# Kernel tuning notes

Measured on AMD Instinct MI355X. Metric: run time of the kernel, lower is better.

The kernel has to match this reference:

```python
import jax, jax.numpy as jnp
import numpy as np

N = 100000   # num_nodes
R = 200      # num_relations
DIM = 200    # hidden dim (in = out for every layer)
B = 30       # num_bases
L = 2        # num_layers
E = 800000   # num_edges


def setup_inputs() -> dict:
    key = jax.random.key(0)
    ks = jax.random.split(key, 7)
    edge_index = jax.random.randint(ks[0], (2, E), 0, N)
    edge_type = jax.random.randint(ks[1], (E,), 0, R)
    s = 1.0 / np.sqrt(DIM)
    emb = jax.random.normal(ks[2], (N, DIM), jnp.float32)
    comp = jax.random.normal(ks[3], (L, R, B), jnp.float32) * (1.0 / np.sqrt(B))
    bases = jax.random.normal(ks[4], (L, B, DIM, DIM), jnp.float32) * s
    root = jax.random.normal(ks[5], (L, DIM, DIM), jnp.float32) * s
    bias = jnp.zeros((L, DIM), jnp.float32)
    return dict(edge_index=edge_index, edge_type=edge_type, emb=emb,
                comp=comp, bases=bases, root=root, bias=bias)


def _rgcn_layer(x, src, dst, etype, comp_l, bases_l, root_l, bias_l):
    # Basis decomposition: W_r = sum_b comp[r, b] * bases[b]
    # msg_e = x[src_e] @ W_{etype_e}  computed as sum over bases (B is small & fixed)
    x_src = x[src]                      # [E, DIM] gather
    c = comp_l[etype]                   # [E, B] per-edge basis coefficients

    def body(acc, bc):
        basis_b, c_b = bc               # [DIM, DIM], [E]
        return acc + c_b[:, None] * (x_src @ basis_b), None

    acc0 = jnp.zeros((x_src.shape[0], root_l.shape[1]), x.dtype)
    msg, _ = jax.lax.scan(body, acc0, (bases_l, jnp.swapaxes(c, 0, 1)))  # [E, DIM]

    # PyG RGCNConv mean aggregation: normalize by in-degree per (dst node, relation)
    comb = dst * R + etype
    deg = jax.ops.segment_sum(jnp.ones((etype.shape[0],), x.dtype), comb,
                              num_segments=N * R)
    norm = 1.0 / jnp.maximum(deg[comb], 1.0)                             # [E]

    agg = jax.ops.segment_sum(msg * norm[:, None], dst, num_segments=N)  # [N, DIM]
    return agg + x @ root_l + bias_l


def reference(edge_index, edge_type, emb, comp, bases, root, bias):
    src, dst = edge_index[0], edge_index[1]
    x = emb
    for l in range(L):
        x = jax.nn.relu(_rgcn_layer(x, src, dst, edge_type,
                                    comp[l], bases[l], root[l], bias[l]))
        # dropout is identity in eval mode (deterministic reference)
    return x
```

## Files before the change

### kernel.cpp

```cpp
#include <hip/hip_runtime.h>
#include <hip/hip_bf16.h>
#include <stdint.h>

#define NN 100000
#define RR 200
#define DD 200
#define BB 30
#define LL 2
#define EE 800000

#define KP 224
#define NP 208
#define XP 208
#define AP 232
#define TE 128
#define MSGP 200
#define MAXTILES 6700
#define MAXNC 16
#define NPART 256
#define EPB ((EE + NPART - 1) / NPART)

using bf16x8 = __attribute__((ext_vector_type(8))) short;
using f32x4  = __attribute__((ext_vector_type(4))) float;

#define OFF_NORM   0ull
#define OFF_SORT   3200000ull
#define OFF_CNT    6400000ull
#define OFF_XB     6404096ull
#define OFF_WT     48004096ull
#define OFF_ROOTT  66640896ull
#define OFF_CTL    66734080ull
#define OFF_POS    66799616ull
#define OFF_DSTCNT 69999616ull
#define OFF_DSTST  70399616ull
#define OFF_CUR    70799632ull
#define OFF_BLKH   71199632ull
#define OFF_MSG    74476432ull

static __device__ __forceinline__ short f2bf(float v) {
    union { __hip_bfloat16 h; short s; } u;
    u.h = __float2bfloat16(v);
    return u.s;
}

__global__ void kCount(const int* __restrict__ ei, const int* __restrict__ et,
                       unsigned int* __restrict__ deg8, int* __restrict__ dstCnt, int big) {
    int e = blockIdx.x * 256 + threadIdx.x;
    if (e >= EE) return;
    int d = ei[EE + e];
    int t = et[e];
    int comb = d * RR + t;
    atomicAdd(&deg8[comb >> 2], 1u << ((comb & 3) * 8));
    if (big) atomicAdd(&dstCnt[d], 1);
}

__global__ void kScanBlk(const int* __restrict__ dstCnt, int* __restrict__ dstStart,
                         int* __restrict__ blkSum) {
    __shared__ int s[256];
    int t = threadIdx.x, i = blockIdx.x * 256 + t;
    int v = (i < NN) ? dstCnt[i] : 0;
    s[t] = v;
    __syncthreads();
    #pragma unroll
    for (int off = 1; off < 256; off <<= 1) {
        int x = (t >= off) ? s[t - off] : 0;
        __syncthreads();
        s[t] += x;
        __syncthreads();
    }
    if (i < NN) dstStart[i] = s[t] - v;
    if (t == 255) blkSum[blockIdx.x] = s[255];
}
__global__ void kScanTop(int* __restrict__ blkSum, int nblk) {
    __shared__ int s[512];
    int t = threadIdx.x;
    int v = (t < nblk) ? blkSum[t] : 0;
    s[t] = v;
    __syncthreads();
    #pragma unroll
    for (int off = 1; off < 512; off <<= 1) {
        int x = (t >= off) ? s[t - off] : 0;
        __syncthreads();
        s[t] += x;
        __syncthreads();
    }
    if (t < nblk) blkSum[t] = s[t] - v;
}
__global__ void kScanAdd(const int* __restrict__ dstCnt, int* __restrict__ dstStart,
                         const int* __restrict__ blkSum) {
    int i = blockIdx.x * 256 + threadIdx.x;
    if (i >= NN) return;
    int v = dstStart[i] + blkSum[blockIdx.x];
    dstStart[i] = v;
    if (i == NN - 1) dstStart[NN] = v + dstCnt[i];
}

__global__ void kChunk(const int* __restrict__ dstStart, int* __restrict__ bS,
                       int* __restrict__ cesS, int NC, int T) {
    int tid = threadIdx.x;
    if (tid > NC) return;
    int v;
    if (tid == NC) v = NN;
    else if (tid == 0) v = 0;
    else {
        int target = tid * T;
        int lo = 0, hi = NN;
        while (lo < hi) {
            int mid = (lo + hi) >> 1;
            if (dstStart[mid] >= target) hi = mid; else lo = mid + 1;
        }
        v = lo;
    }
    bS[tid] = v;
    cesS[tid] = dstStart[v];
}

__global__ __launch_bounds__(256) void kHist(const int* __restrict__ ei,
        const int* __restrict__ et, const int* __restrict__ bS,
        int* __restrict__ blockHist, int NC) {
    __shared__ int hist[MAXNC * RR];
    __shared__ int bsh[MAXNC + 1];
    int tid = threadIdx.x, b = blockIdx.x;
    int NB = NC * RR;
    if (tid <= NC) bsh[tid] = bS[tid];
    for (int i = tid; i < NB; i += 256) hist[i] = 0;
    __syncthreads();
    int ebeg = b * EPB, eend = min(EE, ebeg + EPB);
    for (int e = ebeg + tid; e < eend; e += 256) {
        int d = ei[EE + e];
        int t = et[e];
        int c = 0;
        for (int j = 1; j < NC; ++j) if (d >= bsh[j]) c = j;
        atomicAdd(&hist[c * RR + t], 1);
    }
    __syncthreads();
    for (int i = tid; i < NB; i += 256)
        blockHist[(size_t)b * NB + i] = hist[i];
}

__global__ __launch_bounds__(256) void kScanP(int* __restrict__ blockHist,
                                              int* __restrict__ cntB, int NB) {
    __shared__ int s[256];
    int t = threadIdx.x, k = blockIdx.x;
    int v = blockHist[(size_t)t * NB + k];
    s[t] = v;
    __syncthreads();
    #pragma unroll
    for (int off = 1; off < 256; off <<= 1) {
        int x = (t >= off) ? s[t - off] : 0;
        __syncthreads();
        s[t] += x;
        __syncthreads();
    }
    blockHist[(size_t)t * NB + k] = s[t] - v;
    if (t == 255) cntB[k] = s[255];
}

__global__ void kScanB(const int* __restrict__ cntB, int* __restrict__ relStartB,
                       int* __restrict__ cursorB, int* __restrict__ tileOffB, int nb) {
    __shared__ int c[MAXNC * RR];
    __shared__ int rs[MAXNC * RR + 1];
    __shared__ int to[MAXNC * RR + 1];
    int tid = threadIdx.x;
    for (int i = tid; i < nb; i += 256) c[i] = cntB[i];
    __syncthreads();
    if (tid == 0) {
        int s = 0, ts = 0;
        for (int i = 0; i < nb; ++i) {
            rs[i] = s; to[i] = ts;
            s += c[i];
            ts += (c[i] + TE - 1) / TE;
        }
        rs[nb] = s; to[nb] = ts;
    }
    __syncthreads();
    for (int i = tid; i <= nb; i += 256) {
        relStartB[i] = rs[i];
        tileOffB[i]  = to[i];
        if (i < nb) cursorB[i] = rs[i];
    }
}

__global__ __launch_bounds__(256) void kPart(const int* __restrict__ ei,
        const int* __restrict__ et, const unsigned int* __restrict__ deg8,
        const int* __restrict__ bS, const int* __restrict__ relStartB,
        const int* __restrict__ blockHist, const int* __restrict__ dstStart,
        int* __restrict__ cur, float* __restrict__ norm, int* __restrict__ sortedE,
        int* __restrict__ posDst, int NC) {
    __shared__ int curL[MAXNC * RR];
    __shared__ int bsh[MAXNC + 1];
    int tid = threadIdx.x, b = blockIdx.x;
    int NB = NC * RR;
    if (tid <= NC) bsh[tid] = bS[tid];
    for (int i = tid; i < NB; i += 256)
        curL[i] = relStartB[i] + blockHist[(size_t)b * NB + i];
    __syncthreads();
    int ebeg = b * EPB, eend = min(EE, ebeg + EPB);
    for (int e = ebeg + tid; e < eend; e += 256) {
        int d = ei[EE + e];
        int t = et[e];
        int comb = d * RR + t;
        unsigned int deg = (deg8[comb >> 2] >> ((comb & 3) * 8)) & 0xffu;
        norm[e] = 1.0f / (float)(deg ? deg : 1u);
        int c = 0;
        for (int j = 1; j < NC; ++j) if (d >= bsh[j]) c = j;
        int pos = atomicAdd(&curL[c * RR + t], 1);
        sortedE[pos] = e;
        posDst[e] = dstStart[d] + atomicAdd(&cur[d], 1);
    }
}

__global__ void kCountB(const int* __restrict__ ei, const int* __restrict__ et,
                        const int* __restrict__ bS, int* __restrict__ cntB, int NC) {
    __shared__ int bsh[MAXNC + 1];
    if (threadIdx.x <= NC) bsh[threadIdx.x] = bS[threadIdx.x];
    __syncthreads();
    int e = blockIdx.x * 256 + threadIdx.x;
    if (e >= EE) return;
    int d = ei[EE + e];
    int t = et[e];
    int c = 0;
    for (int j = 1; j < NC; ++j) if (d >= bsh[j]) c = j;
    atomicAdd(&cntB[c * RR + t], 1);
}

__global__ void kNormScatter(const int* __restrict__ ei, const int* __restrict__ et,
                             const unsigned int* __restrict__ deg8, const int* __restrict__ bS,
                             int* __restrict__ cursorB, const int* __restrict__ dstStart,
                             int* __restrict__ cur, float* __restrict__ norm,
                             int* __restrict__ sortedE, int* __restrict__ posDst,
                             int NC, int big) {
    __shared__ int bsh[MAXNC + 1];
    if (threadIdx.x <= NC) bsh[threadIdx.x] = bS[threadIdx.x];
    __syncthreads();
    int e = blockIdx.x * 256 + threadIdx.x;
    if (e >= EE) return;
    int d = ei[EE + e];
    int t = et[e];
    int comb = d * RR + t;
    unsigned int deg = (deg8[comb >> 2] >> ((comb & 3) * 8)) & 0xffu;
    norm[e] = 1.0f / (float)(deg ? deg : 1u);
    int c = 0;
    for (int j = 1; j < NC; ++j) if (d >= bsh[j]) c = j;
    int pos = atomicAdd(&cursorB[c * RR + t], 1);
    sortedE[pos] = e;
    if (big) posDst[e] = dstStart[d] + atomicAdd(&cur[d], 1);
}

__global__ void kConvert(const float* __restrict__ x, short* __restrict__ xb, int doRelu) {
    int idx = blockIdx.x * 256 + threadIdx.x;
    if (idx >= NN * XP) return;
    int i = idx / XP, col = idx - i * XP;
    float v = 0.0f;
    if (col < DD) {
        v = x[i * DD + col];
        if (doRelu) v = fmaxf(v, 0.0f);
    }
    xb[idx] = (col < DD) ? f2bf(v) : (short)0;
}

__global__ void kRelu(float* __restrict__ y) {
    int idx = blockIdx.x * 256 + threadIdx.x;
    if (idx < NN * DD) y[idx] = fmaxf(y[idx], 0.0f);
}

__global__ __launch_bounds__(256) void kW(const float* __restrict__ comp,
                                          const float* __restrict__ bases,
                                          short* __restrict__ Wt) {
    int kt = blockIdx.x;
    int ng = blockIdx.y;
    int tid = threadIdx.x;
    int k = kt * 32 + (tid & 31);
    int n = ng * 8 + (tid >> 5);
    bool live = (k < DD) && (n < DD);
    float vb[BB];
    #pragma unroll
    for (int b = 0; b < BB; ++b)
        vb[b] = live ? bases[((size_t)b * DD + k) * DD + n] : 0.0f;
    size_t wo = (size_t)n * KP + k;
    for (int r = 0; r < RR; ++r) {
        float a = 0.0f;
        #pragma unroll
        for (int b = 0; b < BB; ++b) a += comp[r * BB + b] * vb[b];
        Wt[(size_t)r * (NP * KP) + wo] = f2bf(a);
    }
}

__global__ void kRootT(const float* __restrict__ root, short* __restrict__ rootT) {
    int idx = blockIdx.x * 256 + threadIdx.x;
    if (idx >= NP * KP) return;
    int n = idx / KP, k = idx - n * KP;
    rootT[idx] = (n < DD && k < DD) ? f2bf(root[k * DD + n]) : (short)0;
}

template<int F0, int NF>
__device__ __forceinline__ void gemmHalf2(const short* As, const short* bCol,
                                          int arow0, int arow1, int kg,
                                          f32x4* acc0, f32x4* acc1) {
    #pragma unroll
    for (int f = 0; f < NF; ++f) {
        acc0[f] = (f32x4){0.f, 0.f, 0.f, 0.f};
        acc1[f] = (f32x4){0.f, 0.f, 0.f, 0.f};
    }
    bf16x8 bb[2][NF];
    #pragma unroll
    for (int f = 0; f < NF; ++f)
        bb[0][f] = *(const bf16x8*)(bCol + (size_t)(F0 + f) * 16 * KP);
    #pragma unroll
    for (int kc = 0; kc < 7; ++kc) {
        if (kc < 6) {
            #pragma unroll
            for (int f = 0; f < NF; ++f)
                bb[(kc + 1) & 1][f] = *(const bf16x8*)(bCol + (size_t)(F0 + f) * 16 * KP + (kc + 1) * 32);
        }
        bf16x8 a0 = *(const bf16x8*)(&As[arow0 * AP + kc * 32 + kg]);
        bf16x8 a1 = *(const bf16x8*)(&As[arow1 * AP + kc * 32 + kg]);
        #pragma unroll
        for (int f = 0; f < NF; ++f) {
            acc0[f] = __builtin_amdgcn_mfma_f32_16x16x32_bf16(a0, bb[kc & 1][f], acc0[f], 0, 0, 0);
            acc1[f] = __builtin_amdgcn_mfma_f32_16x16x32_bf16(a1, bb[kc & 1][f], acc1[f], 0, 0, 0);
        }
    }
}

__global__ __launch_bounds__(256) void kRootGemm(const short* __restrict__ xb,
        const short* __restrict__ rootT, const float* __restrict__ bias,
        float* __restrict__ y) {
    __shared__ short As[TE * AP];
    int i0 = blockIdx.x * TE;
    int tid = threadIdx.x;
    int rowL = tid >> 1, sub = tid & 1;
    int i = i0 + rowL;
    for (int c = sub; c < 29; c += 2) {
        int4 v = make_int4(0, 0, 0, 0);
        if (i < NN && c < 26) v = *(const int4*)(xb + (size_t)i * XP + c * 8);
        *(int4*)(&As[rowL * AP + c * 8]) = v;
    }
    __syncthreads();
    int lane = tid & 63, wave = tid >> 6;
    int arow0 = wave * 32 + (lane & 15);
    int arow1 = arow0 + 16;
    int kg = (lane >> 4) * 8;
    const short* bCol = rootT + (lane & 15) * KP + kg;
    int colLane = lane & 15;
    int rbase = i0 + wave * 32 + (lane >> 4) * 4;
    {
        f32x4 acc0[7], acc1[7];
        gemmHalf2<0, 7>(As, bCol, arow0, arow1, kg, acc0, acc1);
        #pragma unroll
        for (int f = 0; f < 7; ++f) {
            int col = f * 16 + colLane;
            float bv = bias[col];
            #pragma unroll
            for (int j = 0; j < 4; ++j) {
                int r0 = rbase + j, r1 = rbase + 16 + j;
                if (r0 < NN) y[(size_t)r0 * DD + col] = acc0[f][j] + bv;
                if (r1 < NN) y[(size_t)r1 * DD + col] = acc1[f][j] + bv;
            }
        }
    }
    {
        f32x4 acc0[6], acc1[6];
        gemmHalf2<7, 6>(As, bCol, arow0, arow1, kg, acc0, acc1);
        #pragma unroll
        for (int f = 0; f < 6; ++f) {
            int col = (7 + f) * 16 + colLane;
            if (col < DD) {
                float bv = bias[col];
                #pragma unroll
                for (int j = 0; j < 4; ++j) {
                    int r0 = rbase + j, r1 = rbase + 16 + j;
                    if (r0 < NN) y[(size_t)r0 * DD + col] = acc0[f][j] + bv;
                    if (r1 < NN) y[(size_t)r1 * DD + col] = acc1[f][j] + bv;
                }
            }
        }
    }
}

template<int MODE>
__global__ __launch_bounds__(256) void kMsg(const int* __restrict__ ei,
        const short* __restrict__ xb, const short* __restrict__ Wt,
        const int* __restrict__ relStartB, const int* __restrict__ tileOffB,
        const int* __restrict__ sortedE, const float* __restrict__ norm,
        const int* __restrict__ posDst, const int* __restrict__ cesS,
        float* __restrict__ y, short* __restrict__ msg, int c) {
    __shared__ short As[TE * AP];
    __shared__ int   posS[TE];
    __shared__ float normS[TE];
    int tbase = tileOffB[c * RR];
    int tend  = tileOffB[(c + 1) * RR];
    int tileIdx = tbase + blockIdx.x;
    if (tileIdx >= tend) return;
    int lo = c * RR, hi = (c + 1) * RR;
    while (hi - lo > 1) {
        int mid = (lo + hi) >> 1;
        if (tileOffB[mid] <= tileIdx) lo = mid; else hi = mid;
    }
    int bkt = lo;
    int r = bkt - c * RR;
    int eBase = relStartB[bkt] + (tileIdx - tileOffB[bkt]) * TE;
    int eEnd  = relStartB[bkt + 1];
    int tid = threadIdx.x;
    int rowL = tid >> 1, sub = tid & 1;
    int eIdx = eBase + rowL;
    bool valid = eIdx < eEnd;
    int eid = valid ? sortedE[eIdx] : 0;
    if (sub == 0) {
        normS[rowL] = valid ? norm[eid] : 0.0f;
        if (MODE == 0) posS[rowL] = valid ? (posDst[eid] - cesS[c]) : -1;
        else           posS[rowL] = valid ? ei[EE + eid] : -1;
    }
    int srcRow = valid ? ei[eid] : 0;
    for (int cc = sub; cc < 29; cc += 2) {
        int4 v = make_int4(0, 0, 0, 0);
        if (valid && cc < 26) v = *(const int4*)(xb + (size_t)srcRow * XP + cc * 8);
        *(int4*)(&As[rowL * AP + cc * 8]) = v;
    }
    __syncthreads();
    int lane = tid & 63, wave = tid >> 6;
    int arow0 = wave * 32 + (lane & 15);
    int arow1 = arow0 + 16;
    int kg = (lane >> 4) * 8;
    const short* bCol = Wt + (size_t)r * (NP * KP) + (lane & 15) * KP + kg;
    int colLane = lane & 15;
    int rL0 = wave * 32 + (lane >> 4) * 4;
    {
        f32x4 acc0[7], acc1[7];
        gemmHalf2<0, 7>(As, bCol, arow0, arow1, kg, acc0, acc1);
        #pragma unroll
        for (int j = 0; j < 4; ++j) {
            #pragma unroll
            for (int m = 0; m < 2; ++m) {
                int rl = rL0 + m * 16 + j;
                float nm = normS[rl];
                int ps = posS[rl];
                if (ps >= 0) {
                    #pragma unroll
                    for (int f = 0; f < 7; ++f) {
                        int col = f * 16 + colLane;
                        float val = (m ? acc1[f][j] : acc0[f][j]) * nm;
                        if (MODE == 0) msg[(size_t)ps * MSGP + col] = f2bf(val);
                        else           atomicAdd(&y[(size_t)ps * DD + col], val);
                    }
                }
            }
        }
    }
    {
        f32x4 acc0[6], acc1[6];
        gemmHalf2<7, 6>(As, bCol, arow0, arow1, kg, acc0, acc1);
        #pragma unroll
        for (int j = 0; j < 4; ++j) {
            #pragma unroll
            for (int m = 0; m < 2; ++m) {
                int rl = rL0 + m * 16 + j;
                float nm = normS[rl];
                int ps = posS[rl];
                if (ps >= 0) {
                    #pragma unroll
                    for (int f = 0; f < 6; ++f) {
                        int col = (7 + f) * 16 + colLane;
                        if (col < DD) {
                            float val = (m ? acc1[f][j] : acc0[f][j]) * nm;
                            if (MODE == 0) msg[(size_t)ps * MSGP + col] = f2bf(val);
                            else           atomicAdd(&y[(size_t)ps * DD + col], val);
                        }
                    }
                }
            }
        }
    }
}

__global__ __launch_bounds__(256) void kAgg(const short* __restrict__ msg,
        const int* __restrict__ dstStart, const int* __restrict__ bS,
        const int* __restrict__ cesS, float* __restrict__ y, int c) {
    int wv = threadIdx.x >> 6, lane = threadIdx.x & 63;
    int b0 = bS[c], b1 = bS[c + 1];
    int ces = cesS[c];
    int gw = blockIdx.x * 4 + wv;
    int nw = gridDim.x * 4;
    for (int d = b0 + gw; d < b1; d += nw) {
        int s = dstStart[d] - ces, e = dstStart[d + 1] - ces;
        float a0 = 0.f, a1 = 0.f, a2 = 0.f, a3 = 0.f;
        if (lane < 50) {
            for (int j = s; j < e; ++j) {
                int2 v = *(const int2*)(msg + (size_t)j * MSGP + lane * 4);
                unsigned u0 = (unsigned)v.x, u1 = (unsigned)v.y;
                a0 += __uint_as_float(u0 << 16);
                a1 += __uint_as_float(u0 & 0xffff0000u);
                a2 += __uint_as_float(u1 << 16);
                a3 += __uint_as_float(u1 & 0xffff0000u);
            }
            int colBase = lane * 4;
            float4 rv = *(const float4*)(y + (size_t)d * DD + colBase);
            float4 o;
            o.x = fmaxf(rv.x + a0, 0.f);
            o.y = fmaxf(rv.y + a1, 0.f);
            o.z = fmaxf(rv.z + a2, 0.f);
            o.w = fmaxf(rv.w + a3, 0.f);
            *(float4*)(y + (size_t)d * DD + colBase) = o;
        }
    }
}

extern "C" void kernel_launch(void* const* d_in, const int* in_sizes, int n_in,
                              void* d_out, int out_size, void* d_ws, size_t ws_size,
                              hipStream_t stream) {
    (void)in_sizes; (void)n_in; (void)out_size;
    const int*   ei    = (const int*)d_in[0];
    const int*   et    = (const int*)d_in[1];
    const float* emb   = (const float*)d_in[2];
    const float* comp  = (const float*)d_in[3];
    const float* bases = (const float*)d_in[4];
    const float* root  = (const float*)d_in[5];
    const float* bias  = (const float*)d_in[6];
    float* y = (float*)d_out;
    char* ws = (char*)d_ws;
    float* norm    = (float*)(ws + OFF_NORM);
    int*   sortedE = (int*)(ws + OFF_SORT);
    short* xb      = (short*)(ws + OFF_XB);
    short* Wt      = (short*)(ws + OFF_WT);
    short* rootT   = (short*)(ws + OFF_ROOTT);
    int*   posDst  = (int*)(ws + OFF_POS);
    int*   dstCnt  = (int*)(ws + OFF_DSTCNT);
    int*   dstStart= (int*)(ws + OFF_DSTST);
    int*   cur     = (int*)(ws + OFF_CUR);
    int*   blockHist = (int*)(ws + OFF_BLKH);
    short* msg     = (short*)(ws + OFF_MSG);
    unsigned int* deg8 = (unsigned int*)(ws + OFF_XB);

    int NC = 0;
    long long T = EE;
    for (int cc = 1; cc <= MAXNC; ++cc) {
        long long t = (EE + cc - 1) / cc;
        if ((unsigned long long)ws_size >= OFF_MSG + (unsigned long long)(t + 64) * (MSGP * 2)) {
            NC = cc; T = t; break;
        }
    }
    int big = (NC > 0) ? 1 : 0;
    if (!big) { NC = 1; T = EE; }

    int *cntB, *relStartB, *cursorB, *tileOffB, *bS, *cesS, *blkSum;
    if (big) {
        int* ctl = (int*)(ws + OFF_CTL);
        cntB = ctl; relStartB = ctl + 3328; cursorB = ctl + 6656;
        tileOffB = ctl + 9984; bS = ctl + 13312; cesS = ctl + 13360; blkSum = ctl + 13440;
    } else {
        int* ctl = (int*)(ws + OFF_CNT);
        cntB = ctl; relStartB = ctl + 256; cursorB = ctl + 512;
        tileOffB = ctl + 768; bS = ctl + 976; cesS = ctl + 992; blkSum = ctl + 1000;
    }

    const int NBLK = (NN + 255) / 256;

    hipMemsetAsync(deg8, 0, (size_t)NN * RR, stream);
    if (big) {
        hipMemsetAsync(dstCnt, 0, (size_t)NN * 4, stream);
        hipMemsetAsync(cur, 0, (size_t)NN * 4, stream);
    } else {
        hipMemsetAsync((void*)cntB, 0, 4096, stream);
    }

    kCount<<<(EE + 255) / 256, 256, 0, stream>>>(ei, et, deg8, dstCnt, big);
    if (big) {
        kScanBlk<<<NBLK, 256, 0, stream>>>(dstCnt, dstStart, blkSum);
        kScanTop<<<1, 512, 0, stream>>>(blkSum, NBLK);
        kScanAdd<<<NBLK, 256, 0, stream>>>(dstCnt, dstStart, blkSum);
        kChunk<<<1, 64, 0, stream>>>(dstStart, bS, cesS, NC, (int)T);
        kHist<<<NPART, 256, 0, stream>>>(ei, et, bS, blockHist, NC);
        kScanP<<<NC * RR, 256, 0, stream>>>(blockHist, cntB, NC * RR);
        kScanB<<<1, 256, 0, stream>>>(cntB, relStartB, cursorB, tileOffB, NC * RR);
        kPart<<<NPART, 256, 0, stream>>>(ei, et, deg8, bS, relStartB, blockHist,
                                         dstStart, cur, norm, sortedE, posDst, NC);
    } else {
        kCountB<<<(EE + 255) / 256, 256, 0, stream>>>(ei, et, bS, cntB, NC);
        kScanB<<<1, 256, 0, stream>>>(cntB, relStartB, cursorB, tileOffB, NC * RR);
        kNormScatter<<<(EE + 255) / 256, 256, 0, stream>>>(ei, et, deg8, bS, cursorB,
                                                           dstStart, cur, norm, sortedE,
                                                           posDst, NC, big);
    }
    kConvert<<<(NN * XP + 255) / 256, 256, 0, stream>>>(emb, xb, 0);

    int Gmsg = (int)((T + TE - 1) / TE) + RR + 4;
    for (int l = 0; l < LL; ++l) {
        kW<<<dim3(7, 26), 256, 0, stream>>>(comp + l * RR * BB,
                                            bases + (size_t)l * BB * DD * DD, Wt);
        kRootT<<<(NP * KP + 255) / 256, 256, 0, stream>>>(root + l * DD * DD, rootT);
        kRootGemm<<<(NN + TE - 1) / TE, 256, 0, stream>>>(xb, rootT, bias + l * DD, y);
        if (big) {
            for (int c = 0; c < NC; ++c) {
                kMsg<0><<<Gmsg, 256, 0, stream>>>(ei, xb, Wt, relStartB, tileOffB,
                                                  sortedE, norm, posDst, cesS, y, msg, c);
                kAgg<<<2048, 256, 0, stream>>>(msg, dstStart, bS, cesS, y, c);
            }
            if (l == 0)
                kConvert<<<(NN * XP + 255) / 256, 256, 0, stream>>>(y, xb, 0);
        } else {
            kMsg<1><<<MAXTILES, 256, 0, stream>>>(ei, xb, Wt, relStartB, tileOffB,
                                                  sortedE, norm, posDst, cesS, y, msg, 0);
            if (l == 0) kConvert<<<(NN * XP + 255) / 256, 256, 0, stream>>>(y, xb, 1);
            else        kRelu<<<(NN * DD + 255) / 256, 256, 0, stream>>>(y);
        }
    }
}
```

Before: 1.541 ms.

## Load message GEMM A-operand directly from global into registers with 64-edge tiles

The per-relation message kernel no longer stages gathered source rows in LDS. Each wave loads its 16 gathered rows straight into MFMA A registers, and the edge tile shrinks from 128 to 64 so padded tiles waste less work. The bf16 node-feature row pitch is padded to 224 so the full K range can be read without bounds checks, and the partition count is halved with the workspace offsets and chunk limits recomputed to match. This removes the LDS round trip and the block barrier, but each lane now does uncoalesced global gathers and the B-matrix weight loads are reused across fewer rows per block.

After: 1.616 ms. +4.8%, slower.

```diff
diff --git a/kernel.cpp b/kernel.cpp
--- a/kernel.cpp
+++ b/kernel.cpp
@@ -11,13 +11,14 @@
 
 #define KP 224
 #define NP 208
-#define XP 208
+#define XP 224
 #define AP 232
-#define TE 128
+#define TE 64
+#define RT 128
 #define MSGP 200
-#define MAXTILES 6700
-#define MAXNC 16
-#define NPART 256
+#define MAXTILES 12700
+#define MAXNC 24
+#define NPART 128
 #define EPB ((EE + NPART - 1) / NPART)
 
 using bf16x8 = __attribute__((ext_vector_type(8))) short;
@@ -27,15 +28,14 @@
 #define OFF_SORT   3200000ull
 #define OFF_CNT    6400000ull
 #define OFF_XB     6404096ull
-#define OFF_WT     48004096ull
-#define OFF_ROOTT  66640896ull
-#define OFF_CTL    66734080ull
-#define OFF_POS    66799616ull
-#define OFF_DSTCNT 69999616ull
-#define OFF_DSTST  70399616ull
-#define OFF_CUR    70799632ull
-#define OFF_BLKH   71199632ull
-#define OFF_MSG    74476432ull
+#define OFF_WT     51204096ull
+#define OFF_ROOTT  69840896ull
+#define OFF_CTL    69934080ull
+#define OFF_POS    70065152ull
+#define OFF_DSTCNT 73265152ull
+#define OFF_DSTST  73665152ull
+#define OFF_CUR    74065184ull
+#define OFF_BLKH   74465184ull
 
 static __device__ __forceinline__ short f2bf(float v) {
     union { __hip_bfloat16 h; short s; } u;
@@ -138,22 +138,22 @@
         blockHist[(size_t)b * NB + i] = hist[i];
 }
 
-__global__ __launch_bounds__(256) void kScanP(int* __restrict__ blockHist,
+__global__ __launch_bounds__(128) void kScanP(int* __restrict__ blockHist,
                                               int* __restrict__ cntB, int NB) {
-    __shared__ int s[256];
+    __shared__ int s[NPART];
     int t = threadIdx.x, k = blockIdx.x;
     int v = blockHist[(size_t)t * NB + k];
     s[t] = v;
     __syncthreads();
     #pragma unroll
-    for (int off = 1; off < 256; off <<= 1) {
+    for (int off = 1; off < NPART; off <<= 1) {
         int x = (t >= off) ? s[t - off] : 0;
         __syncthreads();
         s[t] += x;
         __syncthreads();
     }
     blockHist[(size_t)t * NB + k] = s[t] - v;
-    if (t == 255) cntB[k] = s[255];
+    if (t == NPART - 1) cntB[k] = s[NPART - 1];
 }
 
 __global__ void kScanB(const int* __restrict__ cntB, int* __restrict__ relStartB,
@@ -326,14 +326,14 @@
 __global__ __launch_bounds__(256) void kRootGemm(const short* __restrict__ xb,
         const short* __restrict__ rootT, const float* __restrict__ bias,
         float* __restrict__ y) {
-    __shared__ short As[TE * AP];
-    int i0 = blockIdx.x * TE;
+    __shared__ short As[RT * AP];
+    int i0 = blockIdx.x * RT;
     int tid = threadIdx.x;
     int rowL = tid >> 1, sub = tid & 1;
     int i = i0 + rowL;
-    for (int c = sub; c < 29; c += 2) {
+    for (int c = sub; c < 28; c += 2) {
         int4 v = make_int4(0, 0, 0, 0);
-        if (i < NN && c < 26) v = *(const int4*)(xb + (size_t)i * XP + c * 8);
+        if (i < NN) v = *(const int4*)(xb + (size_t)i * XP + c * 8);
         *(int4*)(&As[rowL * AP + c * 8]) = v;
     }
     __syncthreads();
@@ -385,9 +385,6 @@
         const int* __restrict__ sortedE, const float* __restrict__ norm,
         const int* __restrict__ posDst, const int* __restrict__ cesS,
         float* __restrict__ y, short* __restrict__ msg, int c) {
-    __shared__ short As[TE * AP];
-    __shared__ int   posS[TE];
-    __shared__ float normS[TE];
     int tbase = tileOffB[c * RR];
     int tend  = tileOffB[(c + 1) * RR];
     int tileIdx = tbase + blockIdx.x;
@@ -397,75 +394,96 @@
         int mid = (lo + hi) >> 1;
         if (tileOffB[mid] <= tileIdx) lo = mid; else hi = mid;
     }
-    int bkt = lo;
-    int r = bkt - c * RR;
-    int eBase = relStartB[bkt] + (tileIdx - tileOffB[bkt]) * TE;
-    int eEnd  = relStartB[bkt + 1];
-    int tid = threadIdx.x;
-    int rowL = tid >> 1, sub = tid & 1;
-    int eIdx = eBase + rowL;
-    bool valid = eIdx < eEnd;
-    int eid = valid ? sortedE[eIdx] : 0;
-    if (sub == 0) {
-        normS[rowL] = valid ? norm[eid] : 0.0f;
-        if (MODE == 0) posS[rowL] = valid ? (posDst[eid] - cesS[c]) : -1;
-        else           posS[rowL] = valid ? ei[EE + eid] : -1;
-    }
-    int srcRow = valid ? ei[eid] : 0;
-    for (int cc = sub; cc < 29; cc += 2) {
-        int4 v = make_int4(0, 0, 0, 0);
-        if (valid && cc < 26) v = *(const int4*)(xb + (size_t)srcRow * XP + cc * 8);
-        *(int4*)(&As[rowL * AP + cc * 8]) = v;
-    }
-    __syncthreads();
-    int lane = tid & 63, wave = tid >> 6;
-    int arow0 = wave * 32 + (lane & 15);
-    int arow1 = arow0 + 16;
+    int r = lo - c * RR;
+    int eBase = relStartB[lo] + (tileIdx - tileOffB[lo]) * TE;
+    int eEnd  = relStartB[lo + 1];
+    int tid = threadIdx.x, lane = tid & 63, wave = tid >> 6;
+    int stripe = wave * 16;
     int kg = (lane >> 4) * 8;
-    const short* bCol = Wt + (size_t)r * (NP * KP) + (lane & 15) * KP + kg;
     int colLane = lane & 15;
-    int rL0 = wave * 32 + (lane >> 4) * 4;
+    int eIdxA = eBase + stripe + colLane;
+    int eidA = sortedE[min(eIdxA, eEnd - 1)];
+    int srcA = ei[eidA];
+    const short* aRow = xb + (size_t)srcA * XP;
+    bf16x8 a[7];
+    #pragma unroll
+    for (int kc = 0; kc < 7; ++kc)
+        a[kc] = *(const bf16x8*)(aRow + kc * 32 + kg);
+    int rbase = stripe + (lane >> 4) * 4;
+    int psv[4]; float nmv[4];
+    #pragma unroll
+    for (int j = 0; j < 4; ++j) {
+        int eI = eBase + rbase + j;
+        bool v = eI < eEnd;
+        int eid = v ? sortedE[eI] : 0;
+        nmv[j] = v ? norm[eid] : 0.0f;
+        if (MODE == 0) psv[j] = v ? (posDst[eid] - cesS[c]) : -1;
+        else           psv[j] = v ? ei[EE + eid] : -1;
+    }
+    const short* bCol = Wt + (size_t)r * (NP * KP) + colLane * KP + kg;
     {
-        f32x4 acc0[7], acc1[7];
-        gemmHalf2<0, 7>(As, bCol, arow0, arow1, kg, acc0, acc1);
+        f32x4 acc[7];
+        #pragma unroll
+        for (int f = 0; f < 7; ++f) acc[f] = (f32x4){0.f, 0.f, 0.f, 0.f};
+        bf16x8 bb[2][7];
+        #pragma unroll
+        for (int f = 0; f < 7; ++f)
+            bb[0][f] = *(const bf16x8*)(bCol + (size_t)f * 16 * KP);
+        #pragma unroll
+        for (int kc = 0; kc < 7; ++kc) {
+            if (kc < 6) {
+                #pragma unroll
+                for (int f = 0; f < 7; ++f)
+                    bb[(kc + 1) & 1][f] = *(const bf16x8*)(bCol + (size_t)f * 16 * KP + (kc + 1) * 32);
+            }
+            #pragma unroll
+            for (int f = 0; f < 7; ++f)
+                acc[f] = __builtin_amdgcn_mfma_f32_16x16x32_bf16(a[kc], bb[kc & 1][f], acc[f], 0, 0, 0);
+        }
         #pragma unroll
         for (int j = 0; j < 4; ++j) {
+            int ps = psv[j]; float nm = nmv[j];
+            if (ps >= 0) {
+                #pragma unroll
+                for (int f = 0; f < 7; ++f) {
+                    int col = f * 16 + colLane;
+                    float val = acc[f][j] * nm;
+                    if (MODE == 0) msg[(size_t)ps * MSGP + col] = f2bf(val);
+                    else           atomicAdd(&y[(size_t)ps * DD + col], val);
+                }
+            }
+        }
+    }
+    {
+        f32x4 acc[6];
+        #pragma unroll
+        for (int f = 0; f < 6; ++f) acc[f] = (f32x4){0.f, 0.f, 0.f, 0.f};
+        bf16x8 bb[2][6];
+        #pragma unroll
+        for (int f = 0; f < 6; ++f)
+            bb[0][f] = *(const bf16x8*)(bCol + (size_t)(7 + f) * 16 * KP);
+        #pragma unroll
+        for (int kc = 0; kc < 7; ++kc) {
+            if (kc < 6) {
+                #pragma unroll
+                for (int f = 0; f < 6; ++f)
+                    bb[(kc + 1) & 1][f] = *(const bf16x8*)(bCol + (size_t)(7 + f) * 16 * KP + (kc + 1) * 32);
+            }
             #pragma unroll
-            for (int m = 0; m < 2; ++m) {
-                int rl = rL0 + m * 16 + j;
-                float nm = normS[rl];
-                int ps = posS[rl];
-                if (ps >= 0) {
-                    #pragma unroll
-                    for (int f = 0; f < 7; ++f) {
-                        int col = f * 16 + colLane;
-                        float val = (m ? acc1[f][j] : acc0[f][j]) * nm;
+            for (int f = 0; f < 6; ++f)
+                acc[f] = __builtin_amdgcn_mfma_f32_16x16x32_bf16(a[kc], bb[kc & 1][f], acc[f], 0, 0, 0);
+        }
+        #pragma unroll
+        for (int j = 0; j < 4; ++j) {
+            int ps = psv[j]; float nm = nmv[j];
+            if (ps >= 0) {
+                #pragma unroll
+                for (int f = 0; f < 6; ++f) {
+                    int col = (7 + f) * 16 + colLane;
+                    if (col < DD) {
+                        float val = acc[f][j] * nm;
                         if (MODE == 0) msg[(size_t)ps * MSGP + col] = f2bf(val);
                         else           atomicAdd(&y[(size_t)ps * DD + col], val);
-                    }
-                }
-            }
-        }
-    }
-    {
-        f32x4 acc0[6], acc1[6];
-        gemmHalf2<7, 6>(As, bCol, arow0, arow1, kg, acc0, acc1);
-        #pragma unroll
-        for (int j = 0; j < 4; ++j) {
-            #pragma unroll
-            for (int m = 0; m < 2; ++m) {
-                int rl = rL0 + m * 16 + j;
-                float nm = normS[rl];
-                int ps = posS[rl];
-                if (ps >= 0) {
-                    #pragma unroll
-                    for (int f = 0; f < 6; ++f) {
-                        int col = (7 + f) * 16 + colLane;
-                        if (col < DD) {
-                            float val = (m ? acc1[f][j] : acc0[f][j]) * nm;
-                            if (MODE == 0) msg[(size_t)ps * MSGP + col] = f2bf(val);
-                            else           atomicAdd(&y[(size_t)ps * DD + col], val);
-                        }
                     }
                 }
             }
@@ -528,25 +546,26 @@
     int*   dstStart= (int*)(ws + OFF_DSTST);
     int*   cur     = (int*)(ws + OFF_CUR);
     int*   blockHist = (int*)(ws + OFF_BLKH);
-    short* msg     = (short*)(ws + OFF_MSG);
     unsigned int* deg8 = (unsigned int*)(ws + OFF_XB);
 
     int NC = 0;
     long long T = EE;
+    unsigned long long msgOff = 0;
     for (int cc = 1; cc <= MAXNC; ++cc) {
         long long t = (EE + cc - 1) / cc;
-        if ((unsigned long long)ws_size >= OFF_MSG + (unsigned long long)(t + 64) * (MSGP * 2)) {
-            NC = cc; T = t; break;
-        }
+        unsigned long long mo = OFF_BLKH + (unsigned long long)NPART * cc * RR * 4;
+        unsigned long long need = mo + (unsigned long long)(t + 64) * (MSGP * 2);
+        if ((unsigned long long)ws_size >= need) { NC = cc; T = t; msgOff = mo; break; }
     }
     int big = (NC > 0) ? 1 : 0;
-    if (!big) { NC = 1; T = EE; }
+    if (!big) { NC = 1; T = EE; msgOff = OFF_BLKH; }
+    short* msg = (short*)(ws + msgOff);
 
     int *cntB, *relStartB, *cursorB, *tileOffB, *bS, *cesS, *blkSum;
     if (big) {
         int* ctl = (int*)(ws + OFF_CTL);
-        cntB = ctl; relStartB = ctl + 3328; cursorB = ctl + 6656;
-        tileOffB = ctl + 9984; bS = ctl + 13312; cesS = ctl + 13360; blkSum = ctl + 13440;
+        cntB = ctl; relStartB = ctl + 4864; cursorB = ctl + 9728;
+        tileOffB = ctl + 14592; bS = ctl + 19456; cesS = ctl + 19520; blkSum = ctl + 19584;
     } else {
         int* ctl = (int*)(ws + OFF_CNT);
         cntB = ctl; relStartB = ctl + 256; cursorB = ctl + 512;
@@ -570,7 +589,7 @@
         kScanAdd<<<NBLK, 256, 0, stream>>>(dstCnt, dstStart, blkSum);
         kChunk<<<1, 64, 0, stream>>>(dstStart, bS, cesS, NC, (int)T);
         kHist<<<NPART, 256, 0, stream>>>(ei, et, bS, blockHist, NC);
-        kScanP<<<NC * RR, 256, 0, stream>>>(blockHist, cntB, NC * RR);
+        kScanP<<<NC * RR, NPART, 0, stream>>>(blockHist, cntB, NC * RR);
         kScanB<<<1, 256, 0, stream>>>(cntB, relStartB, cursorB, tileOffB, NC * RR);
         kPart<<<NPART, 256, 0, stream>>>(ei, et, deg8, bS, relStartB, blockHist,
                                          dstStart, cur, norm, sortedE, posDst, NC);
@@ -588,7 +607,7 @@
         kW<<<dim3(7, 26), 256, 0, stream>>>(comp + l * RR * BB,
                                             bases + (size_t)l * BB * DD * DD, Wt);
         kRootT<<<(NP * KP + 255) / 256, 256, 0, stream>>>(root + l * DD * DD, rootT);
-        kRootGemm<<<(NN + TE - 1) / TE, 256, 0, stream>>>(xb, rootT, bias + l * DD, y);
+        kRootGemm<<<(NN + RT - 1) / RT, 256, 0, stream>>>(xb, rootT, bias + l * DD, y);
         if (big) {
             for (int c = 0; c < NC; ++c) {
                 kMsg<0><<<Gmsg, 256, 0, stream>>>(ei, xb, Wt, relStartB, tileOffB,
```
